# Optimization experiments

Measured on AMD Instinct MI355X. Metric: run time of the kernel, lower is better.

The kernel has to match this reference:

```python
import jax, jax.numpy as jnp
import numpy as np

S, B, H = 2048, 2, 1024
NH = 16
HD = H // NH
EPS = 1e-5


def _ln(z, w, b):
    m = jnp.mean(z, axis=-1, keepdims=True)
    v = jnp.mean(jnp.square(z - m), axis=-1, keepdims=True)
    return (z - m) * jax.lax.rsqrt(v + EPS) * w + b


def setup_inputs() -> dict:
    key = jax.random.key(0)
    ks = jax.random.split(key, 8)
    std = 0.02
    return {
        "x": jax.random.normal(ks[0], (S, B, H), dtype=jnp.float32),
        "ln1_w": jnp.ones((H,), jnp.float32),
        "ln1_b": jnp.zeros((H,), jnp.float32),
        "w_qkv": jax.random.normal(ks[1], (3 * H, H), jnp.float32) * std,
        "b_qkv": jnp.zeros((3 * H,), jnp.float32),
        "w_proj": jax.random.normal(ks[2], (H, H), jnp.float32) * std,
        "b_proj": jnp.zeros((H,), jnp.float32),
        "ln2_w": jnp.ones((H,), jnp.float32),
        "ln2_b": jnp.zeros((H,), jnp.float32),
        "w_fc1": jax.random.normal(ks[3], (4 * H, H), jnp.float32) * std,
        "b_fc1": jnp.zeros((4 * H,), jnp.float32),
        "w_fc2": jax.random.normal(ks[4], (H, 4 * H), jnp.float32) * std,
        "b_fc2": jnp.zeros((H,), jnp.float32),
    }


def reference(x, ln1_w, ln1_b, w_qkv, b_qkv, w_proj, b_proj,
              ln2_w, ln2_b, w_fc1, b_fc1, w_fc2, b_fc2):
    s, b, h = x.shape
    # --- LayerNormLinear: LN then fused QKV projection ---
    residual = x
    qkv = _ln(x, ln1_w, ln1_b) @ w_qkv.T + b_qkv            # [S, B, 3H]
    # per-head interleaved packing: [S, B, NH, 3*HD] then split on last dim
    qkv = qkv.reshape(s, b, NH, 3 * HD).transpose(1, 2, 0, 3)  # [B, NH, S, 3HD]
    q, k, v = jnp.split(qkv, 3, axis=3)                      # each [B, NH, S, HD]
    # --- naive causal attention with full SxS scores ---
    scores = jnp.einsum("bhsd,bhtd->bhst", q, k) * (HD ** -0.5)
    causal = jnp.triu(jnp.ones((s, s), dtype=bool), k=1)
    scores = jnp.where(causal, -jnp.inf, scores)
    attn = jax.nn.softmax(scores, axis=-1)                   # [B, NH, S, S]
    out = jnp.einsum("bhst,bhtd->bhsd", attn, v)             # [B, NH, S, HD]
    out = out.transpose(0, 2, 1, 3).reshape(b, s, h).transpose(1, 0, 2)  # [S, B, H]
    out = out @ w_proj.T + b_proj
    x = residual + out
    # --- LayerNormMLP: LN -> fc1 -> gelu(tanh) -> fc2, residual ---
    residual = x
    hmid = jax.nn.gelu(_ln(x, ln2_w, ln2_b) @ w_fc1.T + b_fc1, approximate=True)
    x = residual + (hmid @ w_fc2.T + b_fc2)
    return x
```

## Files before the change

kernel.cpp:

```cpp
#include <hip/hip_runtime.h>
#include <math.h>

#define S_LEN 2048
#define B_SZ 2
#define NHEAD 16
#define HDIM 64
#define H_DIM 1024
#define M_ROWS (S_LEN * B_SZ)
#define LN_EPS 1e-5f
#define KSTR 72
#define SCL 0.18033688011112042f

typedef __attribute__((ext_vector_type(4))) float f32x4;
typedef __attribute__((ext_vector_type(8))) short short8;
typedef __attribute__((ext_vector_type(8))) unsigned short u16x8;
typedef __attribute__((ext_vector_type(4))) unsigned short u16x4;
typedef __attribute__((ext_vector_type(2))) unsigned short u16x2;

typedef __attribute__((address_space(3))) unsigned int lds_u32;
typedef const __attribute__((address_space(1))) unsigned int glb_u32;

#define ASM_VMCNT(N) asm volatile("s_waitcnt vmcnt(" #N ")" ::: "memory")
#define ASM_LGKM0()  asm volatile("s_waitcnt lgkmcnt(0)" ::: "memory")

__device__ __forceinline__ float bf2f(unsigned short u) {
    return __uint_as_float(((unsigned int)u) << 16);
}
__device__ __forceinline__ unsigned short f2bf(float f) {
    unsigned int u = __float_as_uint(f);
    return (unsigned short)((u + 0x7fffu + ((u >> 16) & 1u)) >> 16);
}

__global__ __launch_bounds__(256) void cast_all(const float* __restrict__ wqkv,
                                                const float* __restrict__ wproj,
                                                const float* __restrict__ wfc1,
                                                const float* __restrict__ wfc2,
                                                unsigned short* __restrict__ oqkv,
                                                unsigned short* __restrict__ oproj,
                                                unsigned short* __restrict__ ofc1,
                                                unsigned short* __restrict__ ofc2) {
    const int i = blockIdx.x * 256 + threadIdx.x;
    const float* src; unsigned short* dst; int off;
    if (i < 786432)       { src = wqkv;  dst = oqkv;  off = i; }
    else if (i < 1048576) { src = wproj; dst = oproj; off = i - 786432; }
    else if (i < 2097152) { src = wfc1;  dst = ofc1;  off = i - 1048576; }
    else                  { src = wfc2;  dst = ofc2;  off = i - 2097152; }
    f32x4 v = ((const f32x4*)src)[off];
    u16x4 o;
    o.x = f2bf(v.x); o.y = f2bf(v.y); o.z = f2bf(v.z); o.w = f2bf(v.w);
    ((u16x4*)dst)[off] = o;
}

__global__ __launch_bounds__(256) void ln_bf16(const float* __restrict__ x,
                                               const float* __restrict__ w,
                                               const float* __restrict__ b,
                                               unsigned short* __restrict__ y) {
    const int m = blockIdx.x;
    const int tid = threadIdx.x;
    const float* row = x + (size_t)m * H_DIM;

    float4 v = ((const float4*)row)[tid];
    float s  = v.x + v.y + v.z + v.w;
    float ss = v.x * v.x + v.y * v.y + v.z * v.z + v.w * v.w;

    __shared__ float rs[4], rss[4], stats[2];
    const int wave = tid >> 6, lane = tid & 63;
    for (int off = 32; off; off >>= 1) {
        s  += __shfl_down(s, off);
        ss += __shfl_down(ss, off);
    }
    if (lane == 0) { rs[wave] = s; rss[wave] = ss; }
    __syncthreads();
    if (tid == 0) {
        float S = rs[0] + rs[1] + rs[2] + rs[3];
        float SS = rss[0] + rss[1] + rss[2] + rss[3];
        float mean = S * (1.0f / H_DIM);
        float var = SS * (1.0f / H_DIM) - mean * mean;
        stats[0] = mean;
        stats[1] = rsqrtf(var + LN_EPS);
    }
    __syncthreads();
    const float mean = stats[0], inv = stats[1];
    float4 wv = ((const float4*)w)[tid];
    float4 bv = ((const float4*)b)[tid];
    u16x4 o;
    o.x = f2bf((v.x - mean) * inv * wv.x + bv.x);
    o.y = f2bf((v.y - mean) * inv * wv.y + bv.y);
    o.z = f2bf((v.z - mean) * inv * wv.z + bv.z);
    o.w = f2bf((v.w - mean) * inv * wv.w + bv.w);
    ((u16x4*)(y + (size_t)m * H_DIM))[tid] = o;
}

template <int EPI, bool BF_OUT, int TN>
__global__ __launch_bounds__(256) void gemm_mfma(const unsigned short* __restrict__ A,
                                                 const unsigned short* __restrict__ B,
                                                 const float* __restrict__ bias,
                                                 const float* __restrict__ resid,
                                                 void* __restrict__ Cout,
                                                 int M, int N, int K) {
    constexpr int NJ  = TN / 32;
    constexpr int ANI = 4;
    constexpr int BNI = TN / 32;
    constexpr int NBUF = (TN == 128) ? 2 : 3;
    __shared__ __attribute__((aligned(16))) unsigned short As[NBUF][128 * 64];
    __shared__ __attribute__((aligned(16))) unsigned short Bs[NBUF][TN * 64];

    const int tid = threadIdx.x;
    const int wid = tid >> 6;
    const int ln  = tid & 63;
    const int quad = ln >> 4;
    const int mr   = ln & 15;
    const int wm = (wid >> 1) * 64;
    const int wn = (wid & 1) * (TN / 2);

    const int mb = M >> 7;
    const int stripe = mb >> 3;
    const int xcd = blockIdx.x & 7;
    const int local = blockIdx.x >> 3;
    const int m0 = (xcd * stripe + (local % stripe)) << 7;
    const int n0 = (local / stripe) * TN;

    const int lr = ln >> 3, lc = ln & 7;
    const size_t Kb = (size_t)K * 2;
    const char* gA = (const char*)A + (size_t)(m0 + wid * 32 + lr) * Kb
                     + (size_t)((lc << 4) ^ (lr << 4));
    const int bwr = (TN == 128) ? wid * 32 : wid * 16;
    const char* gB = (const char*)B + (size_t)(n0 + bwr + lr) * Kb
                     + (size_t)((lc << 4) ^ (lr << 4));

    auto stage = [&](int kt, int buf) {
        const char* pa = gA + (size_t)kt * 128;
        unsigned int* la = (unsigned int*)&As[buf][0] + wid * (ANI * 256);
#pragma unroll
        for (int i = 0; i < ANI; i++)
            __builtin_amdgcn_global_load_lds((glb_u32*)(pa + (size_t)i * 8 * Kb),
                                             (lds_u32*)(la + i * 256), 16, 0, 0);
        const char* pb = gB + (size_t)kt * 128;
        unsigned int* lb = (unsigned int*)&Bs[buf][0] + wid * (BNI * 256);
#pragma unroll
        for (int i = 0; i < BNI; i++)
            __builtin_amdgcn_global_load_lds((glb_u32*)(pb + (size_t)i * 8 * Kb),
                                             (lds_u32*)(lb + i * 256), 16, 0, 0);
    };

    const f32x4 zero = {0.f, 0.f, 0.f, 0.f};
    f32x4 acc[4][NJ];
#pragma unroll
    for (int i = 0; i < 4; i++)
#pragma unroll
        for (int j = 0; j < NJ; j++) acc[i][j] = zero;

    const int swz = (mr & 7) << 3;
    auto compute = [&](const unsigned short* As_, const unsigned short* Bs_) {
#pragma unroll
        for (int h = 0; h < 2; h++) {
            short8 af[4], bfr[NJ];
#pragma unroll
            for (int i = 0; i < 4; i++)
                af[i] = *(const short8*)(As_ + (wm + i * 16 + mr) * 64
                                             + ((h * 32 + quad * 8) ^ swz));
#pragma unroll
            for (int j = 0; j < NJ; j++)
                bfr[j] = *(const short8*)(Bs_ + (wn + j * 16 + mr) * 64
                                              + ((h * 32 + quad * 8) ^ swz));
#pragma unroll
            for (int i = 0; i < 4; i++)
#pragma unroll
                for (int j = 0; j < NJ; j++)
                    acc[i][j] = __builtin_amdgcn_mfma_f32_16x16x32_bf16(bfr[j], af[i], acc[i][j], 0, 0, 0);
        }
    };

    const int nt = K >> 6;
    stage(0, 0);
    stage(1, 1);
    if (NBUF == 3) stage(2, 2);

    int cb = 0;
    for (int kt = 0; kt < nt; kt++) {
        if (NBUF == 3) {
            if (kt + 2 < nt)      ASM_VMCNT(12);
            else if (kt + 1 < nt) ASM_VMCNT(6);
            else                  ASM_VMCNT(0);
        } else {
            if (kt + 1 < nt)      ASM_VMCNT(8);
            else                  ASM_VMCNT(0);
        }
        __builtin_amdgcn_s_barrier();
        __builtin_amdgcn_sched_barrier(0);
        compute(&As[cb][0], &Bs[cb][0]);
        __builtin_amdgcn_sched_barrier(0);
        __builtin_amdgcn_s_barrier();
        if (kt + NBUF < nt) stage(kt + NBUF, cb);
        cb = (cb + 1 == NBUF) ? 0 : cb + 1;
    }

    f32x4 bias4[NJ];
#pragma unroll
    for (int j = 0; j < NJ; j++)
        bias4[j] = *(const f32x4*)(bias + n0 + wn + j * 16 + quad * 4);

#pragma unroll
    for (int i = 0; i < 4; i++) {
        const int m = m0 + wm + i * 16 + mr;
#pragma unroll
        for (int j = 0; j < NJ; j++) {
            const int nb = n0 + wn + j * 16 + quad * 4;
            f32x4 v = acc[i][j] + bias4[j];
            if (EPI == 1) v += *(const f32x4*)(resid + (size_t)m * N + nb);
            if (EPI == 2) {
#pragma unroll
                for (int r = 0; r < 4; r++) {
                    const float t = v[r];
                    const float u = t + 0.044715f * t * t * t;
                    const float e = exp2f(2.3022112f * u);
                    v[r] = t - t / (e + 1.0f);
                }
            }
            if (BF_OUT) {
                u16x4 pk;
                pk.x = f2bf(v.x); pk.y = f2bf(v.y); pk.z = f2bf(v.z); pk.w = f2bf(v.w);
                *(u16x4*)((unsigned short*)Cout + (size_t)m * N + nb) = pk;
            } else {
                *(f32x4*)((float*)Cout + (size_t)m * N + nb) = v;
            }
        }
    }
}

template <int EPI, bool BF_OUT>
__global__ __launch_bounds__(512, 1) void gemm_8p(const unsigned short* __restrict__ A,
                                                  const unsigned short* __restrict__ B,
                                                  const float* __restrict__ bias,
                                                  const float* __restrict__ resid,
                                                  void* __restrict__ Cout,
                                                  int M, int N, int K) {
    constexpr int SLOT = 256 * 32 * 2;
    __shared__ __attribute__((aligned(16))) unsigned short Ls[4 * SLOT];

    const int tid = threadIdx.x;
    const int wid = tid >> 6;
    const int ln  = tid & 63;
    const int quad = ln >> 4;
    const int mr   = ln & 15;
    const int wr = wid >> 2;
    const int wc = wid & 3;

    const int nm = M >> 8;
    const int stripe = nm >> 3;
    const int xcd = blockIdx.x & 7;
    const int local = blockIdx.x >> 3;
    const int m0 = (xcd * stripe + (local % stripe)) << 8;
    const int n0 = (local / stripe) << 8;

    const int lr2 = ln >> 2, ch = ln & 3;
    const int sch = ((ch ^ ((lr2 >> 1) & 3)) << 4);
    const size_t Kb = (size_t)K * 2;
    const char* gA = (const char*)A + (size_t)(m0 + wid * 32 + lr2) * Kb + sch;
    const char* gB = (const char*)B + (size_t)(n0 + wid * 32 + lr2) * Kb + sch;

    auto stageA = [&](int kt, int slot) {
        const char* p = gA + (size_t)kt * 64;
        unsigned int* l = (unsigned int*)(Ls + slot * SLOT) + (wid * 32) * 16;
#pragma unroll
        for (int i = 0; i < 2; i++)
            __builtin_amdgcn_global_load_lds((glb_u32*)(p + (size_t)(i * 16) * Kb),
                                             (lds_u32*)(l + i * 256), 16, 0, 0);
    };
    auto stageB = [&](int kt, int slot) {
        const char* p = gB + (size_t)kt * 64;
        unsigned int* l = (unsigned int*)(Ls + slot * SLOT + 256 * 32) + (wid * 32) * 16;
#pragma unroll
        for (int i = 0; i < 2; i++)
            __builtin_amdgcn_global_load_lds((glb_u32*)(p + (size_t)(i * 16) * Kb),
                                             (lds_u32*)(l + i * 256), 16, 0, 0);
    };

    const f32x4 zero = {0.f, 0.f, 0.f, 0.f};
    f32x4 acc[8][4];
#pragma unroll
    for (int i = 0; i < 8; i++)
#pragma unroll
        for (int j = 0; j < 4; j++) acc[i][j] = zero;

    const int swzr = ((mr >> 1) & 3) << 4;

    const int nt = K >> 5;
    stageA(0, 0); stageB(0, 0);
    stageA(1, 1); stageB(1, 1);
    ASM_VMCNT(4);
    __builtin_amdgcn_s_barrier();

    for (int t = 0; t < nt; t++) {
        const int slot = t & 3;
        const int s2 = (t + 2) & 3;
        const unsigned short* sa = Ls + slot * SLOT;
        const unsigned short* sb = sa + 256 * 32;
        short8 af[4], bfr[4];
#pragma unroll
        for (int i = 0; i < 4; i++)
            af[i] = *(const short8*)((const char*)sa
                        + (wr * 128 + i * 16 + mr) * 64 + ((quad << 4) ^ swzr));
#pragma unroll
        for (int j = 0; j < 4; j++)
            bfr[j] = *(const short8*)((const char*)sb
                        + (wc * 64 + j * 16 + mr) * 64 + ((quad << 4) ^ swzr));
        if (t + 2 < nt) stageA(t + 2, s2);
        __builtin_amdgcn_s_barrier();
        ASM_LGKM0();
        __builtin_amdgcn_sched_barrier(0);
        __builtin_amdgcn_s_setprio(1);
#pragma unroll
        for (int i = 0; i < 4; i++)
#pragma unroll
            for (int j = 0; j < 4; j++)
                acc[i][j] = __builtin_amdgcn_mfma_f32_16x16x32_bf16(bfr[j], af[i], acc[i][j], 0, 0, 0);
        __builtin_amdgcn_s_setprio(0);
        __builtin_amdgcn_s_barrier();
#pragma unroll
        for (int i = 0; i < 4; i++)
            af[i] = *(const short8*)((const char*)sa
                        + (wr * 128 + 64 + i * 16 + mr) * 64 + ((quad << 4) ^ swzr));
        if (t + 2 < nt) stageB(t + 2, s2);
        __builtin_amdgcn_s_barrier();
        ASM_LGKM0();
        __builtin_amdgcn_sched_barrier(0);
        __builtin_amdgcn_s_setprio(1);
#pragma unroll
        for (int i = 0; i < 4; i++)
#pragma unroll
            for (int j = 0; j < 4; j++)
                acc[4 + i][j] = __builtin_amdgcn_mfma_f32_16x16x32_bf16(bfr[j], af[i], acc[4 + i][j], 0, 0, 0);
        __builtin_amdgcn_s_setprio(0);
        if (t + 2 < nt) ASM_VMCNT(4);
        else            ASM_VMCNT(0);
        __builtin_amdgcn_s_barrier();
    }

    f32x4 bias4[4];
#pragma unroll
    for (int j = 0; j < 4; j++)
        bias4[j] = *(const f32x4*)(bias + n0 + wc * 64 + j * 16 + quad * 4);

#pragma unroll
    for (int mi = 0; mi < 8; mi++) {
        const int m = m0 + wr * 128 + mi * 16 + mr;
#pragma unroll
        for (int j = 0; j < 4; j++) {
            const int nb = n0 + wc * 64 + j * 16 + quad * 4;
            f32x4 v = acc[mi][j] + bias4[j];
            if (EPI == 1) v += *(const f32x4*)(resid + (size_t)m * N + nb);
            if (EPI == 2) {
#pragma unroll
                for (int r = 0; r < 4; r++) {
                    const float t = v[r];
                    const float u = t + 0.044715f * t * t * t;
                    const float e = exp2f(2.3022112f * u);
                    v[r] = t - t / (e + 1.0f);
                }
            }
            if (BF_OUT) {
                u16x4 pk;
                pk.x = f2bf(v.x); pk.y = f2bf(v.y); pk.z = f2bf(v.z); pk.w = f2bf(v.w);
                *(u16x4*)((unsigned short*)Cout + (size_t)m * N + nb) = pk;
            } else {
                *(f32x4*)((float*)Cout + (size_t)m * N + nb) = v;
            }
        }
    }
}

__global__ __launch_bounds__(256) void attn_mfma(const unsigned short* __restrict__ qkv,
                                                 unsigned short* __restrict__ out) {
    __shared__ __attribute__((aligned(16))) unsigned short Ks[64 * KSTR];
    __shared__ __attribute__((aligned(16))) unsigned short Vs[64 * KSTR];
    __shared__ __attribute__((aligned(16))) unsigned short Ps[64 * KSTR];

    const int tid = threadIdx.x;
    const int wid = tid >> 6;
    const int ln  = tid & 63;
    const int quad = ln >> 4;
    const int mr   = ln & 15;

    const int id = blockIdx.x;
    const int local = id >> 3;
    const int bh = (id & 7) * 4 + (local >> 4);
    const int pa = local & 15;
    const int b  = bh >> 4;
    const int nh = bh & 15;
    const size_t chan = (size_t)nh * 192;

    const int ksr = tid >> 2, ksc = tid & 3;
    const int vt0 = (tid & 31) * 2, vd0 = (tid >> 5) * 8;

    u16x8 kp0, kp1, vp0, vp1;

#pragma unroll
    for (int half = 0; half < 2; half++) {
        const int qt = half ? (31 - pa) : pa;
        const int qb = qt * 64;

        short8 qf0, qf1;
        {
            const int qrow = qb + wid * 16 + mr;
            const unsigned short* gq = qkv + ((size_t)(qrow * 2 + b)) * 3072 + chan + quad * 8;
            qf0 = *(const short8*)gq;
            qf1 = *(const short8*)(gq + 32);
        }

        const f32x4 zero = {0.f, 0.f, 0.f, 0.f};
        f32x4 o[4];
        float ps = 0.f;
#pragma unroll
        for (int d = 0; d < 4; d++) o[d] = zero;

        {
            const unsigned short* gk = qkv + ((size_t)(ksr * 2 + b)) * 3072 + chan + 64 + ksc * 16;
            kp0 = *(const u16x8*)gk;
            kp1 = *(const u16x8*)(gk + 8);
            const unsigned short* gv = qkv + ((size_t)(vt0 * 2 + b)) * 3072 + chan + 128 + vd0;
            vp0 = *(const u16x8*)gv;
            vp1 = *(const u16x8*)(gv + 6144);
        }

        for (int kt = 0; kt <= qt; kt++) {
            __syncthreads();
            *(u16x8*)(Ks + ksr * KSTR + ksc * 16) = kp0;
            *(u16x8*)(Ks + ksr * KSTR + ksc * 16 + 8) = kp1;
#pragma unroll
            for (int j = 0; j < 8; j++) {
                u16x2 pr; pr.x = vp0[j]; pr.y = vp1[j];
                *(u16x2*)(Vs + (vd0 + j) * KSTR + vt0) = pr;
            }
            if (kt < qt) {
                const int nb = (kt + 1) * 64;
                const unsigned short* gk =
                    qkv + ((size_t)((nb + ksr) * 2 + b)) * 3072 + chan + 64 + ksc * 16;
                kp0 = *(const u16x8*)gk;
                kp1 = *(const u16x8*)(gk + 8);
                const unsigned short* gv =
                    qkv + ((size_t)((nb + vt0) * 2 + b)) * 3072 + chan + 128 + vd0;
                vp0 = *(const u16x8*)gv;
                vp1 = *(const u16x8*)(gv + 6144);
            }
            __syncthreads();

            f32x4 sacc[4];
#pragma unroll
            for (int n = 0; n < 4; n++) {
                sacc[n] = zero;
                const unsigned short* kb = Ks + (n * 16 + mr) * KSTR + quad * 8;
                short8 kfr0 = *(const short8*)kb;
                short8 kfr1 = *(const short8*)(kb + 32);
                sacc[n] = __builtin_amdgcn_mfma_f32_16x16x32_bf16(kfr0, qf0, sacc[n], 0, 0, 0);
                sacc[n] = __builtin_amdgcn_mfma_f32_16x16x32_bf16(kfr1, qf1, sacc[n], 0, 0, 0);
            }
            if (kt == qt) {
#pragma unroll
                for (int n = 0; n < 4; n++)
#pragma unroll
                    for (int r = 0; r < 4; r++)
                        if (n * 16 + quad * 4 + r > wid * 16 + mr) sacc[n][r] = -3.0e38f;
            }

            unsigned short* prow = Ps + (wid * 16 + mr) * KSTR + quad * 4;
#pragma unroll
            for (int n = 0; n < 4; n++) {
                u16x4 pk;
#pragma unroll
                for (int r = 0; r < 4; r++) {
                    const float p = exp2f(fminf(sacc[n][r] * SCL, 80.f));
                    ps += p;
                    pk[r] = (unsigned short)(__float_as_uint(p) >> 16);
                }
                *(u16x4*)(prow + n * 16) = pk;
            }

            {
                const unsigned short* pb = Ps + (wid * 16 + mr) * KSTR + quad * 8;
                short8 pa0 = *(const short8*)pb;
                short8 pa1 = *(const short8*)(pb + 32);
#pragma unroll
                for (int d = 0; d < 4; d++) {
                    const unsigned short* vb = Vs + (d * 16 + mr) * KSTR + quad * 8;
                    short8 vf0 = *(const short8*)vb;
                    short8 vf1 = *(const short8*)(vb + 32);
                    o[d] = __builtin_amdgcn_mfma_f32_16x16x32_bf16(vf0, pa0, o[d], 0, 0, 0);
                    o[d] = __builtin_amdgcn_mfma_f32_16x16x32_bf16(vf1, pa1, o[d], 0, 0, 0);
                }
            }
        }

        ps += __shfl_xor(ps, 16);
        ps += __shfl_xor(ps, 32);
        const float inv = 1.0f / ps;
        const int qrow = qb + wid * 16 + mr;
        unsigned short* po = out + ((size_t)(qrow * 2 + b)) * H_DIM + nh * HDIM;
#pragma unroll
        for (int d = 0; d < 4; d++) {
            u16x4 pk;
#pragma unroll
            for (int r = 0; r < 4; r++) pk[r] = f2bf(o[d][r] * inv);
            *(u16x4*)(po + d * 16 + quad * 4) = pk;
        }
    }
}

extern "C" void kernel_launch(void* const* d_in, const int* in_sizes, int n_in,
                              void* d_out, int out_size, void* d_ws, size_t ws_size,
                              hipStream_t stream) {
    const float* x      = (const float*)d_in[0];
    const float* ln1_w  = (const float*)d_in[1];
    const float* ln1_b  = (const float*)d_in[2];
    const float* w_qkv  = (const float*)d_in[3];
    const float* b_qkv  = (const float*)d_in[4];
    const float* w_proj = (const float*)d_in[5];
    const float* b_proj = (const float*)d_in[6];
    const float* ln2_w  = (const float*)d_in[7];
    const float* ln2_b  = (const float*)d_in[8];
    const float* w_fc1  = (const float*)d_in[9];
    const float* b_fc1  = (const float*)d_in[10];
    const float* w_fc2  = (const float*)d_in[11];
    const float* b_fc2  = (const float*)d_in[12];
    float* out = (float*)d_out;

    char* ws = (char*)d_ws;
    unsigned short* wqkv_bf  = (unsigned short*)(ws);
    unsigned short* wproj_bf = (unsigned short*)(ws + ((size_t)6 << 20));
    unsigned short* wfc1_bf  = (unsigned short*)(ws + ((size_t)8 << 20));
    unsigned short* wfc2_bf  = (unsigned short*)(ws + ((size_t)16 << 20));
    unsigned short* ln_buf   = (unsigned short*)(ws + ((size_t)24 << 20));
    unsigned short* qkv_bf   = (unsigned short*)(ws + ((size_t)32 << 20));
    unsigned short* attn_bf  = (unsigned short*)(ws + ((size_t)56 << 20));
    unsigned short* fc1_bf   = (unsigned short*)(ws + ((size_t)32 << 20));

    cast_all<<<12288, 256, 0, stream>>>(w_qkv, w_proj, w_fc1, w_fc2,
                                        wqkv_bf, wproj_bf, wfc1_bf, wfc2_bf);

    ln_bf16<<<M_ROWS, 256, 0, stream>>>(x, ln1_w, ln1_b, ln_buf);
    gemm_8p<0, true><<<192, 512, 0, stream>>>(
        ln_buf, wqkv_bf, b_qkv, nullptr, qkv_bf, M_ROWS, 3072, 1024);
    attn_mfma<<<512, 256, 0, stream>>>(qkv_bf, attn_bf);
    gemm_mfma<1, false, 64><<<512, 256, 0, stream>>>(
        attn_bf, wproj_bf, b_proj, x, out, M_ROWS, 1024, 1024);
    ln_bf16<<<M_ROWS, 256, 0, stream>>>(out, ln2_w, ln2_b, ln_buf);
    gemm_8p<2, true><<<256, 512, 0, stream>>>(
        ln_buf, wfc1_bf, b_fc1, nullptr, fc1_bf, M_ROWS, 4096, 1024);
    gemm_mfma<1, false, 64><<<512, 256, 0, stream>>>(
        fc1_bf, wfc2_bf, b_fc2, out, out, M_ROWS, 1024, 4096);
}
```

Baseline: 339.0 us.

## Replace 256x256 GEMM with 128x128 tiles and add split-K atomic fc2

Swaps the 512-thread 256x256-tile GEMM used for the QKV and fc1 projections for a 256-thread 128x128-tile, double-buffered kernel without LDS swizzling, which raises the block count. It also replaces the fc2 GEMM with a split-K (4-way) kernel that accumulates into the output with float atomics, relying on the output already holding the residual. The split-K path gives more parallelism for the long-K GEMM but adds atomic traffic and makes the summation order nondeterministic. The smaller tiles reuse each loaded tile less and may hit LDS bank conflicts since the swizzle is gone.

```diff
diff --git a/kernel.cpp b/kernel.cpp
--- a/kernel.cpp
+++ b/kernel.cpp
@@ -21,7 +21,6 @@
 typedef const __attribute__((address_space(1))) unsigned int glb_u32;
 
 #define ASM_VMCNT(N) asm volatile("s_waitcnt vmcnt(" #N ")" ::: "memory")
-#define ASM_LGKM0()  asm volatile("s_waitcnt lgkmcnt(0)" ::: "memory")
 
 __device__ __forceinline__ float bf2f(unsigned short u) {
     return __uint_as_float(((unsigned int)u) << 16);
@@ -29,6 +28,9 @@
 __device__ __forceinline__ unsigned short f2bf(float f) {
     unsigned int u = __float_as_uint(f);
     return (unsigned short)((u + 0x7fffu + ((u >> 16) & 1u)) >> 16);
+}
+__device__ __forceinline__ void atomic_add_f32(float* p, float v) {
+    asm volatile("global_atomic_add_f32 %0, %1, off" :: "v"(p), "v"(v) : "memory");
 }
 
 __global__ __launch_bounds__(256) void cast_all(const float* __restrict__ wqkv,
@@ -229,126 +231,96 @@
 }
 
 template <int EPI, bool BF_OUT>
-__global__ __launch_bounds__(512, 1) void gemm_8p(const unsigned short* __restrict__ A,
-                                                  const unsigned short* __restrict__ B,
-                                                  const float* __restrict__ bias,
-                                                  const float* __restrict__ resid,
-                                                  void* __restrict__ Cout,
-                                                  int M, int N, int K) {
-    constexpr int SLOT = 256 * 32 * 2;
-    __shared__ __attribute__((aligned(16))) unsigned short Ls[4 * SLOT];
+__global__ __launch_bounds__(256) void gemm_v8(const unsigned short* __restrict__ A,
+                                               const unsigned short* __restrict__ B,
+                                               const float* __restrict__ bias,
+                                               const float* __restrict__ resid,
+                                               void* __restrict__ Cout,
+                                               int M, int N, int K) {
+    __shared__ __attribute__((aligned(16))) unsigned short As[2][128 * 32];
+    __shared__ __attribute__((aligned(16))) unsigned short Bs[2][128 * 32];
 
     const int tid = threadIdx.x;
     const int wid = tid >> 6;
     const int ln  = tid & 63;
     const int quad = ln >> 4;
     const int mr   = ln & 15;
-    const int wr = wid >> 2;
-    const int wc = wid & 3;
-
-    const int nm = M >> 8;
-    const int stripe = nm >> 3;
+    const int wm = (wid >> 1) * 64;
+    const int wn = (wid & 1) * 64;
+
+    const int stripe = (M >> 7) >> 3;
     const int xcd = blockIdx.x & 7;
     const int local = blockIdx.x >> 3;
-    const int m0 = (xcd * stripe + (local % stripe)) << 8;
-    const int n0 = (local / stripe) << 8;
-
-    const int lr2 = ln >> 2, ch = ln & 3;
-    const int sch = ((ch ^ ((lr2 >> 1) & 3)) << 4);
+    const int m0 = (xcd * stripe + (local % stripe)) << 7;
+    const int n0 = (local / stripe) << 7;
+
+    const int lr = ln >> 2, lc = ln & 3;
     const size_t Kb = (size_t)K * 2;
-    const char* gA = (const char*)A + (size_t)(m0 + wid * 32 + lr2) * Kb + sch;
-    const char* gB = (const char*)B + (size_t)(n0 + wid * 32 + lr2) * Kb + sch;
-
-    auto stageA = [&](int kt, int slot) {
-        const char* p = gA + (size_t)kt * 64;
-        unsigned int* l = (unsigned int*)(Ls + slot * SLOT) + (wid * 32) * 16;
+    const char* gA = (const char*)A + (size_t)(m0 + wid * 16 + lr) * Kb + lc * 16;
+    const char* gB = (const char*)B + (size_t)(n0 + wid * 16 + lr) * Kb + lc * 16;
+
+    auto stage = [&](int kt, int buf) {
+        const char* pa = gA + (size_t)kt * 64;
+        unsigned int* la = (unsigned int*)&As[buf][0] + (wid * 16) * 16;
 #pragma unroll
         for (int i = 0; i < 2; i++)
-            __builtin_amdgcn_global_load_lds((glb_u32*)(p + (size_t)(i * 16) * Kb),
-                                             (lds_u32*)(l + i * 256), 16, 0, 0);
+            __builtin_amdgcn_global_load_lds((glb_u32*)(pa + (size_t)(i * 64) * Kb),
+                                             (lds_u32*)(la + i * 1024), 16, 0, 0);
+        const char* pb = gB + (size_t)kt * 64;
+        unsigned int* lb = (unsigned int*)&Bs[buf][0] + (wid * 16) * 16;
+#pragma unroll
+        for (int i = 0; i < 2; i++)
+            __builtin_amdgcn_global_load_lds((glb_u32*)(pb + (size_t)(i * 64) * Kb),
+                                             (lds_u32*)(lb + i * 1024), 16, 0, 0);
     };
-    auto stageB = [&](int kt, int slot) {
-        const char* p = gB + (size_t)kt * 64;
-        unsigned int* l = (unsigned int*)(Ls + slot * SLOT + 256 * 32) + (wid * 32) * 16;
-#pragma unroll
-        for (int i = 0; i < 2; i++)
-            __builtin_amdgcn_global_load_lds((glb_u32*)(p + (size_t)(i * 16) * Kb),
-                                             (lds_u32*)(l + i * 256), 16, 0, 0);
-    };
 
     const f32x4 zero = {0.f, 0.f, 0.f, 0.f};
-    f32x4 acc[8][4];
-#pragma unroll
-    for (int i = 0; i < 8; i++)
+    f32x4 acc[4][4];
+#pragma unroll
+    for (int i = 0; i < 4; i++)
 #pragma unroll
         for (int j = 0; j < 4; j++) acc[i][j] = zero;
 
-    const int swzr = ((mr >> 1) & 3) << 4;
-
-    const int nt = K >> 5;
-    stageA(0, 0); stageB(0, 0);
-    stageA(1, 1); stageB(1, 1);
-    ASM_VMCNT(4);
-    __builtin_amdgcn_s_barrier();
-
-    for (int t = 0; t < nt; t++) {
-        const int slot = t & 3;
-        const int s2 = (t + 2) & 3;
-        const unsigned short* sa = Ls + slot * SLOT;
-        const unsigned short* sb = sa + 256 * 32;
+    auto compute = [&](const unsigned short* As_, const unsigned short* Bs_) {
         short8 af[4], bfr[4];
 #pragma unroll
         for (int i = 0; i < 4; i++)
-            af[i] = *(const short8*)((const char*)sa
-                        + (wr * 128 + i * 16 + mr) * 64 + ((quad << 4) ^ swzr));
+            af[i] = *(const short8*)(As_ + (wm + i * 16 + mr) * 32 + quad * 8);
 #pragma unroll
         for (int j = 0; j < 4; j++)
-            bfr[j] = *(const short8*)((const char*)sb
-                        + (wc * 64 + j * 16 + mr) * 64 + ((quad << 4) ^ swzr));
-        if (t + 2 < nt) stageA(t + 2, s2);
-        __builtin_amdgcn_s_barrier();
-        ASM_LGKM0();
-        __builtin_amdgcn_sched_barrier(0);
-        __builtin_amdgcn_s_setprio(1);
+            bfr[j] = *(const short8*)(Bs_ + (wn + j * 16 + mr) * 32 + quad * 8);
 #pragma unroll
         for (int i = 0; i < 4; i++)
 #pragma unroll
             for (int j = 0; j < 4; j++)
                 acc[i][j] = __builtin_amdgcn_mfma_f32_16x16x32_bf16(bfr[j], af[i], acc[i][j], 0, 0, 0);
-        __builtin_amdgcn_s_setprio(0);
+    };
+
+    const int nt = K >> 5;
+    stage(0, 0);
+    stage(1, 1);
+    for (int kt = 0; kt < nt; kt++) {
+        if (kt + 1 < nt) ASM_VMCNT(4); else ASM_VMCNT(0);
         __builtin_amdgcn_s_barrier();
-#pragma unroll
-        for (int i = 0; i < 4; i++)
-            af[i] = *(const short8*)((const char*)sa
-                        + (wr * 128 + 64 + i * 16 + mr) * 64 + ((quad << 4) ^ swzr));
-        if (t + 2 < nt) stageB(t + 2, s2);
+        __builtin_amdgcn_sched_barrier(0);
+        compute(&As[kt & 1][0], &Bs[kt & 1][0]);
+        __builtin_amdgcn_sched_barrier(0);
         __builtin_amdgcn_s_barrier();
-        ASM_LGKM0();
-        __builtin_amdgcn_sched_barrier(0);
-        __builtin_amdgcn_s_setprio(1);
-#pragma unroll
-        for (int i = 0; i < 4; i++)
-#pragma unroll
-            for (int j = 0; j < 4; j++)
-                acc[4 + i][j] = __builtin_amdgcn_mfma_f32_16x16x32_bf16(bfr[j], af[i], acc[4 + i][j], 0, 0, 0);
-        __builtin_amdgcn_s_setprio(0);
-        if (t + 2 < nt) ASM_VMCNT(4);
-        else            ASM_VMCNT(0);
-        __builtin_amdgcn_s_barrier();
+        if (kt + 2 < nt) stage(kt + 2, kt & 1);
     }
 
     f32x4 bias4[4];
 #pragma unroll
     for (int j = 0; j < 4; j++)
-        bias4[j] = *(const f32x4*)(bias + n0 + wc * 64 + j * 16 + quad * 4);
-
-#pragma unroll
-    for (int mi = 0; mi < 8; mi++) {
-        const int m = m0 + wr * 128 + mi * 16 + mr;
+        bias4[j] = *(const f32x4*)(bias + n0 + wn + j * 16 + quad * 4);
+
+#pragma unroll
+    for (int i = 0; i < 4; i++) {
+        const int m = m0 + wm + i * 16 + mr;
 #pragma unroll
         for (int j = 0; j < 4; j++) {
-            const int nb = n0 + wc * 64 + j * 16 + quad * 4;
-            f32x4 v = acc[mi][j] + bias4[j];
+            const int nb = n0 + wn + j * 16 + quad * 4;
+            f32x4 v = acc[i][j] + bias4[j];
             if (EPI == 1) v += *(const f32x4*)(resid + (size_t)m * N + nb);
             if (EPI == 2) {
 #pragma unroll
@@ -366,6 +338,108 @@
             } else {
                 *(f32x4*)((float*)Cout + (size_t)m * N + nb) = v;
             }
+        }
+    }
+}
+
+__global__ __launch_bounds__(256) void gemm_sk(const unsigned short* __restrict__ A,
+                                               const unsigned short* __restrict__ B,
+                                               const float* __restrict__ bias,
+                                               float* __restrict__ Out,
+                                               int M, int N, int K, int splits) {
+    __shared__ __attribute__((aligned(16))) unsigned short As[2][128 * 32];
+    __shared__ __attribute__((aligned(16))) unsigned short Bs[2][128 * 32];
+
+    const int tid = threadIdx.x;
+    const int wid = tid >> 6;
+    const int ln  = tid & 63;
+    const int quad = ln >> 4;
+    const int mr   = ln & 15;
+    const int wm = (wid >> 1) * 64;
+    const int wn = (wid & 1) * 64;
+
+    const int stripe = (M >> 7) >> 3;
+    const int xcd = blockIdx.x & 7;
+    const int local = blockIdx.x >> 3;
+    const int m0 = (xcd * stripe + (local % stripe)) << 7;
+    const int rest = local / stripe;
+    const int ntl = N >> 7;
+    const int n0 = (rest % ntl) << 7;
+    const int s  = rest / ntl;
+
+    const int Ks = K / splits;
+    const int lr = ln >> 2, lc = ln & 3;
+    const size_t Kb = (size_t)K * 2;
+    const char* gA = (const char*)A + (size_t)(m0 + wid * 16 + lr) * Kb
+                     + (size_t)s * Ks * 2 + lc * 16;
+    const char* gB = (const char*)B + (size_t)(n0 + wid * 16 + lr) * Kb
+                     + (size_t)s * Ks * 2 + lc * 16;
+
+    auto stage = [&](int kt, int buf) {
+        const char* pa = gA + (size_t)kt * 64;
+        unsigned int* la = (unsigned int*)&As[buf][0] + (wid * 16) * 16;
+#pragma unroll
+        for (int i = 0; i < 2; i++)
+            __builtin_amdgcn_global_load_lds((glb_u32*)(pa + (size_t)(i * 64) * Kb),
+                                             (lds_u32*)(la + i * 1024), 16, 0, 0);
+        const char* pb = gB + (size_t)kt * 64;
+        unsigned int* lb = (unsigned int*)&Bs[buf][0] + (wid * 16) * 16;
+#pragma unroll
+        for (int i = 0; i < 2; i++)
+            __builtin_amdgcn_global_load_lds((glb_u32*)(pb + (size_t)(i * 64) * Kb),
+                                             (lds_u32*)(lb + i * 1024), 16, 0, 0);
+    };
+
+    const f32x4 zero = {0.f, 0.f, 0.f, 0.f};
+    f32x4 acc[4][4];
+#pragma unroll
+    for (int i = 0; i < 4; i++)
+#pragma unroll
+        for (int j = 0; j < 4; j++) acc[i][j] = zero;
+
+    auto compute = [&](const unsigned short* As_, const unsigned short* Bs_) {
+        short8 af[4], bfr[4];
+#pragma unroll
+        for (int i = 0; i < 4; i++)
+            af[i] = *(const short8*)(As_ + (wm + i * 16 + mr) * 32 + quad * 8);
+#pragma unroll
+        for (int j = 0; j < 4; j++)
+            bfr[j] = *(const short8*)(Bs_ + (wn + j * 16 + mr) * 32 + quad * 8);
+#pragma unroll
+        for (int i = 0; i < 4; i++)
+#pragma unroll
+            for (int j = 0; j < 4; j++)
+                acc[i][j] = __builtin_amdgcn_mfma_f32_16x16x32_bf16(bfr[j], af[i], acc[i][j], 0, 0, 0);
+    };
+
+    const int nt = Ks >> 5;
+    stage(0, 0);
+    stage(1, 1);
+    for (int kt = 0; kt < nt; kt++) {
+        if (kt + 1 < nt) ASM_VMCNT(4); else ASM_VMCNT(0);
+        __builtin_amdgcn_s_barrier();
+        __builtin_amdgcn_sched_barrier(0);
+        compute(&As[kt & 1][0], &Bs[kt & 1][0]);
+        __builtin_amdgcn_sched_barrier(0);
+        __builtin_amdgcn_s_barrier();
+        if (kt + 2 < nt) stage(kt + 2, kt & 1);
+    }
+
+    f32x4 bias4[4];
+#pragma unroll
+    for (int j = 0; j < 4; j++)
+        bias4[j] = (s == 0) ? *(const f32x4*)(bias + n0 + wn + j * 16 + quad * 4) : zero;
+
+#pragma unroll
+    for (int i = 0; i < 4; i++) {
+        const int m = m0 + wm + i * 16 + mr;
+#pragma unroll
+        for (int j = 0; j < 4; j++) {
+            const int nb = n0 + wn + j * 16 + quad * 4;
+            f32x4 v = acc[i][j] + bias4[j];
+            float* p = Out + (size_t)m * N + nb;
+#pragma unroll
+            for (int r = 0; r < 4; r++) atomic_add_f32(p + r, v[r]);
         }
     }
 }
@@ -538,14 +612,14 @@
                                         wqkv_bf, wproj_bf, wfc1_bf, wfc2_bf);
 
     ln_bf16<<<M_ROWS, 256, 0, stream>>>(x, ln1_w, ln1_b, ln_buf);
-    gemm_8p<0, true><<<192, 512, 0, stream>>>(
+    gemm_v8<0, true><<<768, 256, 0, stream>>>(
         ln_buf, wqkv_bf, b_qkv, nullptr, qkv_bf, M_ROWS, 3072, 1024);
     attn_mfma<<<512, 256, 0, stream>>>(qkv_bf, attn_bf);
     gemm_mfma<1, false, 64><<<512, 256, 0, stream>>>(
         attn_bf, wproj_bf, b_proj, x, out, M_ROWS, 1024, 1024);
     ln_bf16<<<M_ROWS, 256, 0, stream>>>(out, ln2_w, ln2_b, ln_buf);
-    gemm_8p<2, true><<<256, 512, 0, stream>>>(
+    gemm_v8<2, true><<<1024, 256, 0, stream>>>(
         ln_buf, wfc1_bf, b_fc1, nullptr, fc1_bf, M_ROWS, 4096, 1024);
-    gemm_mfma<1, false, 64><<<512, 256, 0, stream>>>(
-        fc1_bf, wfc2_bf, b_fc2, out, out, M_ROWS, 1024, 4096);
-}
+    gemm_sk<<<1024, 256, 0, stream>>>(
+        fc1_bf, wfc2_bf, b_fc2, out, M_ROWS, 1024, 4096, 4);
+}
```

New measurement: 538.2 us. 58.8% more time.
